# Kernel optimization log

Measured on AMD Instinct MI355X. Metric: run time of the kernel, lower is better.

## Reference

```python
import jax, jax.numpy as jnp
import numpy as np

N, D = 4096, 512
TAU, ALPHA, EPS = 0.2, 0.5, 1e-15
L2_EPS = 1e-12  # F.normalize eps


def setup_inputs() -> dict:
    key = jax.random.key(0)
    ks = jax.random.split(key, 12)
    # xavier_normal_ with gain=1.414 for [D, D] linears
    std = 1.414 * (2.0 / (D + D)) ** 0.5
    xn = lambda k: jax.random.normal(k, (D, D), jnp.float32) * std
    return {
        "z1": jax.random.normal(ks[0], (N, D), jnp.float32),
        "z2": jax.random.normal(ks[1], (N, D), jnp.float32),
        # local projector: Linear -> PReLU -> Linear
        "lw1": xn(ks[2]), "lb1": jnp.zeros((D,), jnp.float32),
        "la": jnp.full((1,), 0.25, jnp.float32),  # PReLU weight (torch default 0.25)
        "lw2": xn(ks[3]), "lb2": jnp.zeros((D,), jnp.float32),
        # global projector
        "gw1": xn(ks[4]), "gb1": jnp.zeros((D,), jnp.float32),
        "ga": jnp.full((1,), 0.25, jnp.float32),
        "gw2": xn(ks[5]), "gb2": jnp.zeros((D,), jnp.float32),
        # discriminator bilinear weight
        "W": xn(ks[6]),
        # binary positive-pair mask [N, N]
        "mask": jax.random.randint(ks[7], (N, N), 0, 2, jnp.int32),
    }


def _prelu(x, a):
    return jnp.where(x >= 0, x, a * x)


def _proj(z, w1, b1, a, w2, b2):
    # nn.Sequential(Linear, PReLU, Linear); torch Linear: z @ W.T + b
    return _prelu(z @ w1.T + b1, a[0]) @ w2.T + b2


def _l2norm(z):
    n = jnp.linalg.norm(z, axis=-1, keepdims=True)
    return z / jnp.maximum(n, L2_EPS)


def _infonce(h1, h2, m, tau):
    a = _l2norm(h1)
    b = _l2norm(h2)
    sim_intra = jnp.exp(a @ a.T / tau)  # [N, N]
    sim_inter = jnp.exp(a @ b.T / tau)  # [N, N]
    num = (sim_inter * m).sum(1)
    den = sim_intra.sum(1) + sim_inter.sum(1) - (sim_intra * m).sum(1)
    return (-jnp.log(num / den)).mean()


def reference(z1, z2, lw1, lb1, la, lw2, lb2, gw1, gb1, ga, gw2, gb2, W, mask):
    m = mask.astype(jnp.float32)
    # local (node-level) InfoNCE through the local projector
    h1 = _proj(z1, lw1, lb1, la, lw2, lb2)
    h2 = _proj(z2, lw1, lb1, la, lw2, lb2)
    local = 0.5 * (_infonce(h1, h2, m, TAU) + _infonce(h2, h1, m.T, TAU))

    # global (DGI-style) loss
    def gloss(pos_z, neg_z):
        s = pos_z.mean(0)                               # readout [D]
        h = _proj(s, gw1, gb1, ga, gw2, gb2)            # global projector [D]
        summ = W @ h                                    # [D]
        d_pos = jax.nn.sigmoid(pos_z @ summ)            # [N]
        d_neg = jax.nn.sigmoid(neg_z @ summ)            # [N]
        pos_loss = -jnp.log(d_pos + EPS).mean()
        neg_loss = -jnp.log(1.0 - d_neg + EPS).mean()
        return 0.5 * (pos_loss + neg_loss)

    glob = 0.5 * (gloss(z1, z2) + gloss(z2, z1))
    return ALPHA * local + (1.0 - ALPHA) * glob
```

## Files before the change

kernel.cpp:

```cpp
#include <hip/hip_runtime.h>
#include <math.h>

#define NN 4096
#define DD 512
#define INV_TAU 5.0f
#define EPSV 1e-15f

typedef unsigned short u16;
typedef __attribute__((ext_vector_type(8))) short short8;
typedef __attribute__((ext_vector_type(4))) float f32x4;

__device__ __forceinline__ void gld16(const void* g, void* l) {
  __builtin_amdgcn_global_load_lds(
      (const __attribute__((address_space(1))) unsigned int*)g,
      (__attribute__((address_space(3))) unsigned int*)l, 16, 0, 0);
}

__device__ __forceinline__ void bar_vm4() {
  asm volatile("s_waitcnt vmcnt(4) lgkmcnt(0)\n\ts_barrier" ::: "memory");
}
__device__ __forceinline__ void bar_vm0() {
  asm volatile("s_waitcnt vmcnt(0) lgkmcnt(0)\n\ts_barrier" ::: "memory");
}

__device__ __forceinline__ float bf2f(u16 u) {
  return __uint_as_float(((unsigned)u) << 16);
}
__device__ __forceinline__ u16 f2bf(float x) {
  unsigned u = __float_as_uint(x);
  u += 0x7fff + ((u >> 16) & 1);
  return (u16)(u >> 16);
}

__device__ __forceinline__ float wave_sum(float v) {
#pragma unroll
  for (int o = 32; o > 0; o >>= 1) v += __shfl_down(v, o, 64);
  return v;
}

__global__ __launch_bounds__(256) void tobf16_2(const float* __restrict__ a,
                                                const float* __restrict__ b,
                                                u16* __restrict__ d,
                                                int n4each) {
  const int i = blockIdx.x * 256 + threadIdx.x;
  const float* s =
      (i < n4each) ? a + (size_t)i * 4 : b + (size_t)(i - n4each) * 4;
  float4 v = *(const float4*)s;
  unsigned long long pk = (unsigned long long)f2bf(v.x) |
                          ((unsigned long long)f2bf(v.y) << 16) |
                          ((unsigned long long)f2bf(v.z) << 32) |
                          ((unsigned long long)f2bf(v.w) << 48);
  *(unsigned long long*)&d[(size_t)i * 4] = pk;
}

template <int ACT>
__global__ __launch_bounds__(256) void gemm_mfma(
    const u16* __restrict__ A, const u16* __restrict__ Bw,
    const float* __restrict__ bias, const float* __restrict__ alpha_p,
    u16* __restrict__ out) {
  __shared__ __align__(16) u16 sh[3 * 2 * 128 * 32];
  const int tid = threadIdx.x, w = tid >> 6, lane = tid & 63;
  const int quad = lane >> 4, m16 = lane & 15;
  const int wi = w >> 1, wj = w & 1;
  const int i0 = blockIdx.y * 128, j0 = blockIdx.x * 128;
  const u16* Ab = A + (size_t)blockIdx.z * ((size_t)NN * DD);
  u16* ob = out + (size_t)blockIdx.z * ((size_t)NN * DD);
  const int roff =
      (m16 >> 1) * 64 + (((((m16 & 1) << 2) | quad) ^ (m16 >> 1)) * 8);
  const int st = (lane & 7) ^ (lane >> 3);
  const int srow = 2 * (lane >> 3) + (st >> 2);
  const int scol = (st & 3) * 8;
  const int p = w >> 1, rh = (w & 1) * 64;
  const u16* gs = p ? Bw : Ab;
  const int gr = (p ? j0 : i0) + rh + srow;
  u16* dst0 = sh + p * 4096 + rh * 32;
  auto stage = [&](int bo, int k) {
    const int kn = k * 32;
#pragma unroll
    for (int rr = 0; rr < 64; rr += 16)
      gld16(&gs[(size_t)(gr + rr) * DD + kn + scol], dst0 + bo + rr * 32);
  };
  stage(0, 0);
  stage(8192, 1);
  bar_vm4();
  f32x4 acc[4][4] = {};
  int ro = 0;
  for (int kc = 0; kc < 16; ++kc) {
    if (kc <= 13) {
      int so = ro + 16384;
      if (so >= 24576) so -= 24576;
      stage(so, kc + 2);
    }
    const u16* As = sh + ro;
    const u16* Bs = sh + ro + 4096;
    short8 ar[4], br[4];
#pragma unroll
    for (int s = 0; s < 4; ++s) {
      ar[s] = *(const short8*)&As[(wi * 64 + s * 16) * 32 + roff];
      br[s] = *(const short8*)&Bs[(wj * 64 + s * 16) * 32 + roff];
    }
    __builtin_amdgcn_s_setprio(1);
#pragma unroll
    for (int si = 0; si < 4; ++si)
#pragma unroll
      for (int sj = 0; sj < 4; ++sj)
        acc[si][sj] = __builtin_amdgcn_mfma_f32_16x16x32_bf16(
            ar[si], br[sj], acc[si][sj], 0, 0, 0);
    __builtin_amdgcn_s_setprio(0);
    if (kc <= 13) bar_vm4();
    else if (kc == 14) bar_vm0();
    ro += 8192;
    if (ro == 24576) ro = 0;
  }
  const float al = ACT ? alpha_p[0] : 0.f;
#pragma unroll
  for (int si = 0; si < 4; ++si)
#pragma unroll
    for (int sj = 0; sj < 4; ++sj) {
      const int col = j0 + wj * 64 + sj * 16 + m16;
      const float bv = bias[col];
#pragma unroll
      for (int r = 0; r < 4; ++r) {
        const int row = i0 + wi * 64 + si * 16 + quad * 4 + r;
        float x = acc[si][sj][r] + bv;
        if (ACT) x = (x >= 0.f) ? x : al * x;
        ob[(size_t)row * DD + col] = f2bf(x);
      }
    }
}

__global__ __launch_bounds__(256) void rownorm_bf16(const u16* __restrict__ h,
                                                    u16* __restrict__ o) {
  const int row = blockIdx.x;
  const int t = threadIdx.x;
  const size_t base = (size_t)row * DD;
  float v0 = bf2f(h[base + t]);
  float v1 = bf2f(h[base + 256 + t]);
  float s = v0 * v0 + v1 * v1;
  s = wave_sum(s);
  __shared__ float wsum[4];
  const int lane = t & 63, wid = t >> 6;
  if (lane == 0) wsum[wid] = s;
  __syncthreads();
  if (t == 0) {
    float tot = wsum[0] + wsum[1] + wsum[2] + wsum[3];
    wsum[0] = 1.f / fmaxf(sqrtf(tot), 1e-12f);
  }
  __syncthreads();
  const float inv = wsum[0];
  o[base + t] = f2bf(v0 * inv);
  o[base + 256 + t] = f2bf(v1 * inv);
}

__global__ __launch_bounds__(512) void sim_mfma(
    const u16* __restrict__ na, const u16* __restrict__ nb,
    const int* __restrict__ mask, float* __restrict__ zb) {
  extern __shared__ __align__(16) u16 shm[];
  const int tid = threadIdx.x;
  const int w = tid >> 6, lane = tid & 63;
  const int quad = lane >> 4, m16 = lane & 15;
  const int ig = w & 3, jh = w >> 2;
  const int i0 = blockIdx.y * 128, j0 = blockIdx.x * 128;
  const int roff =
      (m16 >> 1) * 64 + (((((m16 & 1) << 2) | quad) ^ (m16 >> 1)) * 8);
  const int st = (lane & 7) ^ (lane >> 3);
  const int srow = 2 * (lane >> 3) + (st >> 2);
  const int scol = (st & 3) * 8;
  const int p = w >> 1, rh = (w & 1) * 64;
  const u16* gs = (p & 1) ? nb : na;
  const int gr = ((p < 2) ? i0 : j0) + rh + srow;
  u16* dst0 = shm + p * 4096 + rh * 32;
  auto stage = [&](int bo, int k) {
    const int kn = k * 32;
#pragma unroll
    for (int rr = 0; rr < 64; rr += 16)
      gld16(&gs[(size_t)(gr + rr) * DD + kn + scol], dst0 + bo + rr * 32);
  };
  stage(0, 0);
  stage(16384, 1);
  bar_vm4();
  f32x4 a11[2][4] = {}, a12[2][4] = {}, a22[2][4] = {};
  int ro = 0;
  for (int kc = 0; kc < 16; ++kc) {
    if (kc <= 13) {
      int so = ro + 32768;
      if (so >= 49152) so -= 49152;
      stage(so, kc + 2);
    }
    const u16* Ai = shm + ro;
    const u16* Bi = shm + ro + 4096;
    const u16* Aj = shm + ro + 8192;
    const u16* Bj = shm + ro + 12288;
    short8 ai0 = *(const short8*)&Ai[(ig * 32) * 32 + roff];
    short8 ai1 = *(const short8*)&Ai[(ig * 32 + 16) * 32 + roff];
    short8 bi0 = *(const short8*)&Bi[(ig * 32) * 32 + roff];
    short8 bi1 = *(const short8*)&Bi[(ig * 32 + 16) * 32 + roff];
#pragma unroll
    for (int c = 0; c < 4; ++c) {
      short8 aj = *(const short8*)&Aj[(jh * 64 + c * 16) * 32 + roff];
      short8 bj = *(const short8*)&Bj[(jh * 64 + c * 16) * 32 + roff];
      __builtin_amdgcn_s_setprio(1);
      a11[0][c] = __builtin_amdgcn_mfma_f32_16x16x32_bf16(ai0, aj, a11[0][c], 0, 0, 0);
      a11[1][c] = __builtin_amdgcn_mfma_f32_16x16x32_bf16(ai1, aj, a11[1][c], 0, 0, 0);
      a12[0][c] = __builtin_amdgcn_mfma_f32_16x16x32_bf16(ai0, bj, a12[0][c], 0, 0, 0);
      a12[1][c] = __builtin_amdgcn_mfma_f32_16x16x32_bf16(ai1, bj, a12[1][c], 0, 0, 0);
      a22[0][c] = __builtin_amdgcn_mfma_f32_16x16x32_bf16(bi0, bj, a22[0][c], 0, 0, 0);
      a22[1][c] = __builtin_amdgcn_mfma_f32_16x16x32_bf16(bi1, bj, a22[1][c], 0, 0, 0);
      __builtin_amdgcn_s_setprio(0);
    }
    if (kc <= 13) bar_vm4();
    else if (kc == 14) bar_vm0();
    ro += 16384;
    if (ro == 49152) ro = 0;
  }
  float* rred = (float*)(shm + 16384);
  float* cred = rred + 512;
  rred[tid] = 0.f;
  rred[tid + 512] = 0.f;
  __syncthreads();
  float rs11[2][4] = {}, rm11[2][4] = {}, rs12[2][4] = {}, rm12[2][4] = {};
  float cs12[4] = {}, cm12[4] = {}, cs22[4] = {}, cm22[4] = {};
#pragma unroll
  for (int t = 0; t < 2; ++t)
#pragma unroll
    for (int c = 0; c < 4; ++c) {
      const int gj = j0 + jh * 64 + c * 16 + m16;
#pragma unroll
      for (int r = 0; r < 4; ++r) {
        const int gi = i0 + ig * 32 + t * 16 + quad * 4 + r;
        const float mv = (float)mask[(size_t)gi * NN + gj];
        const float e11 = __expf(a11[t][c][r] * INV_TAU);
        const float e12 = __expf(a12[t][c][r] * INV_TAU);
        const float e22 = __expf(a22[t][c][r] * INV_TAU);
        rs11[t][r] += e11;
        rm11[t][r] += e11 * mv;
        rs12[t][r] += e12;
        rm12[t][r] += e12 * mv;
        cs12[c] += e12;
        cm12[c] += e12 * mv;
        cs22[c] += e22;
        cm22[c] += e22 * mv;
      }
    }
#pragma unroll
  for (int t = 0; t < 2; ++t)
#pragma unroll
    for (int r = 0; r < 4; ++r) {
      float v0 = rs11[t][r], v1 = rm11[t][r], v2 = rs12[t][r], v3 = rm12[t][r];
#pragma unroll
      for (int o = 1; o < 16; o <<= 1) {
        v0 += __shfl_xor(v0, o, 64);
        v1 += __shfl_xor(v1, o, 64);
        v2 += __shfl_xor(v2, o, 64);
        v3 += __shfl_xor(v3, o, 64);
      }
      if (m16 == 0) {
        const int il = ig * 32 + t * 16 + quad * 4 + r;
        atomicAdd(&rred[0 * 128 + il], v0);
        atomicAdd(&rred[1 * 128 + il], v1);
        atomicAdd(&rred[2 * 128 + il], v2);
        atomicAdd(&rred[3 * 128 + il], v3);
      }
    }
#pragma unroll
  for (int c = 0; c < 4; ++c) {
    float v0 = cs12[c], v1 = cm12[c], v2 = cs22[c], v3 = cm22[c];
    v0 += __shfl_xor(v0, 16, 64); v0 += __shfl_xor(v0, 32, 64);
    v1 += __shfl_xor(v1, 16, 64); v1 += __shfl_xor(v1, 32, 64);
    v2 += __shfl_xor(v2, 16, 64); v2 += __shfl_xor(v2, 32, 64);
    v3 += __shfl_xor(v3, 16, 64); v3 += __shfl_xor(v3, 32, 64);
    if (lane < 16) {
      const int jl = jh * 64 + c * 16 + lane;
      atomicAdd(&cred[0 * 128 + jl], v0);
      atomicAdd(&cred[1 * 128 + jl], v1);
      atomicAdd(&cred[2 * 128 + jl], v2);
      atomicAdd(&cred[3 * 128 + jl], v3);
    }
  }
  __syncthreads();
  if (tid < 128) {
#pragma unroll
    for (int q = 0; q < 4; ++q)
      atomicAdd(&zb[q * NN + i0 + tid], rred[q * 128 + tid]);
  } else if (tid < 256) {
    const int jl = tid - 128;
#pragma unroll
    for (int q = 0; q < 4; ++q)
      atomicAdd(&zb[(4 + q) * NN + j0 + jl], cred[q * 128 + jl]);
  }
}

__global__ __launch_bounds__(256) void local_fin(const float* __restrict__ zb,
                                                 float* __restrict__ scal) {
  const int i = blockIdx.x * 256 + threadIdx.x;
  const float r11 = zb[i], r11m = zb[NN + i];
  const float r12 = zb[2 * NN + i], r12m = zb[3 * NN + i];
  const float c12 = zb[4 * NN + i], c12m = zb[5 * NN + i];
  const float c22 = zb[6 * NN + i], c22m = zb[7 * NN + i];
  float l1 = -logf(r12m / (r11 + r12 - r11m));
  float l2 = -logf(c12m / (c22 + c12 - c22m));
  l1 = wave_sum(l1);
  l2 = wave_sum(l2);
  __shared__ float b1[4], b2[4];
  const int lane = threadIdx.x & 63, wid = threadIdx.x >> 6;
  if (lane == 0) { b1[wid] = l1; b2[wid] = l2; }
  __syncthreads();
  if (threadIdx.x == 0) {
    atomicAdd(&scal[0], b1[0] + b1[1] + b1[2] + b1[3]);
    atomicAdd(&scal[1], b2[0] + b2[1] + b2[2] + b2[3]);
  }
}

__global__ __launch_bounds__(256) void colmean(const float* __restrict__ z1,
                                               const float* __restrict__ z2,
                                               float* __restrict__ s1,
                                               float* __restrict__ s2) {
  const int c = blockIdx.x * 256 + threadIdx.x;
  const int r0 = blockIdx.y * 64;
  float a = 0.f, b = 0.f;
  for (int r = r0; r < r0 + 64; ++r) {
    a += z1[(size_t)r * DD + c];
    b += z2[(size_t)r * DD + c];
  }
  atomicAdd(&s1[c], a * (1.f / NN));
  atomicAdd(&s2[c], b * (1.f / NN));
}

__global__ __launch_bounds__(256) void matvec2(
    const float* __restrict__ M, const float* __restrict__ x1,
    const float* __restrict__ x2, const float* __restrict__ bias,
    const float* __restrict__ alpha_p, int act, float* __restrict__ y1,
    float* __restrict__ y2) {
  const float* x = blockIdx.y ? x2 : x1;
  float* y = blockIdx.y ? y2 : y1;
  const int row = (blockIdx.x * 256 + threadIdx.x) >> 6;
  const int lane = threadIdx.x & 63;
  float acc = 0.f;
#pragma unroll
  for (int t = 0; t < 8; ++t)
    acc = fmaf(M[(size_t)row * DD + lane + 64 * t], x[lane + 64 * t], acc);
  acc = wave_sum(acc);
  if (lane == 0) {
    if (bias) acc += bias[row];
    if (act) { const float al = alpha_p[0]; acc = (acc >= 0.f) ? acc : al * acc; }
    y[row] = acc;
  }
}

__global__ __launch_bounds__(256) void logsig2(
    const float* __restrict__ z1, const float* __restrict__ z2,
    const float* __restrict__ sm1, const float* __restrict__ sm2,
    float* __restrict__ scal) {
  const int ch = blockIdx.y;
  const float* z = ch ? z2 : z1;
  const float* sp = ch ? sm2 : sm1;
  const float* sn = ch ? sm1 : sm2;
  float* accP = ch ? &scal[4] : &scal[2];
  float* accN = ch ? &scal[3] : &scal[5];
  const int lane = threadIdx.x & 63;
  const int wid = threadIdx.x >> 6;
  const int row = blockIdx.x * 4 + wid;
  float dp = 0.f, dn = 0.f;
#pragma unroll
  for (int t = 0; t < 8; ++t) {
    const float zv = z[(size_t)row * DD + lane + 64 * t];
    dp = fmaf(zv, sp[lane + 64 * t], dp);
    dn = fmaf(zv, sn[lane + 64 * t], dn);
  }
  dp = wave_sum(dp);
  dn = wave_sum(dn);
  __shared__ float bp[4], bn[4];
  if (lane == 0) {
    const float sg = 1.f / (1.f + __expf(-dp));
    bp[wid] = -logf(sg + EPSV);
    const float sg2 = 1.f / (1.f + __expf(-dn));
    bn[wid] = -logf(1.f - sg2 + EPSV);
  }
  __syncthreads();
  if (threadIdx.x == 0) {
    atomicAdd(accP, bp[0] + bp[1] + bp[2] + bp[3]);
    atomicAdd(accN, bn[0] + bn[1] + bn[2] + bn[3]);
  }
}

__global__ void combine(const float* __restrict__ scal, float* __restrict__ out) {
  const float local = 0.5f * (scal[0] + scal[1]) * (1.f / NN);
  const float glob = 0.25f * (scal[2] + scal[3] + scal[4] + scal[5]) * (1.f / NN);
  out[0] = 0.5f * local + 0.5f * glob;
}

extern "C" void kernel_launch(void* const* d_in, const int* in_sizes, int n_in,
                              void* d_out, int out_size, void* d_ws,
                              size_t ws_size, hipStream_t stream) {
  const float* z1 = (const float*)d_in[0];
  const float* z2 = (const float*)d_in[1];
  const float* lw1 = (const float*)d_in[2];
  const float* lb1 = (const float*)d_in[3];
  const float* la = (const float*)d_in[4];
  const float* lw2 = (const float*)d_in[5];
  const float* lb2 = (const float*)d_in[6];
  const float* gw1 = (const float*)d_in[7];
  const float* gb1 = (const float*)d_in[8];
  const float* ga = (const float*)d_in[9];
  const float* gw2 = (const float*)d_in[10];
  const float* gb2 = (const float*)d_in[11];
  const float* W = (const float*)d_in[12];
  const int* mask = (const int*)d_in[13];
  float* out = (float*)d_out;

  static bool attr_set = false;
  if (!attr_set) {
    (void)hipFuncSetAttribute(reinterpret_cast<const void*>(sim_mfma),
                              hipFuncAttributeMaxDynamicSharedMemorySize,
                              98304);
    attr_set = true;
  }

  const size_t ND = (size_t)NN * DD;
  u16* W1b = (u16*)d_ws;
  u16* W2b = W1b + 512 * 512;
  u16* Ab = W1b + 2 * 512 * 512;
  u16* Bb = Ab + 2 * ND;
  float* zbf = (float*)(Bb + 2 * ND);
  float* s1 = zbf + 8 * NN;
  float* s2 = s1 + DD;
  float* scal = s2 + DD;
  float* t1 = scal + 16;
  float* hg1 = t1 + DD;
  float* summ1 = hg1 + DD;
  float* t2 = summ1 + DD;
  float* hg2 = t2 + DD;
  float* summ2 = hg2 + DD;

  hipMemsetAsync(zbf, 0, (8 * NN + 2 * DD + 16) * sizeof(float), stream);

  dim3 blk(256);
  tobf16_2<<<512, blk, 0, stream>>>(lw1, lw2, W1b, 512 * 512 / 4);
  tobf16_2<<<4096, blk, 0, stream>>>(z1, z2, Ab, (int)(ND / 4));

  dim3 gg(4, 32, 2);
  gemm_mfma<1><<<gg, blk, 0, stream>>>(Ab, W1b, lb1, la, Bb);
  gemm_mfma<0><<<gg, blk, 0, stream>>>(Bb, W2b, lb2, la, Ab);
  rownorm_bf16<<<2 * NN, blk, 0, stream>>>(Ab, Bb);

  sim_mfma<<<dim3(NN / 128, NN / 128), dim3(512), 98304, stream>>>(
      Bb, Bb + ND, mask, zbf);
  local_fin<<<NN / 256, blk, 0, stream>>>(zbf, scal);

  colmean<<<dim3(DD / 256, 64), blk, 0, stream>>>(z1, z2, s1, s2);
  matvec2<<<dim3(DD / 4, 2), blk, 0, stream>>>(gw1, s1, s2, gb1, ga, 1, t1, t2);
  matvec2<<<dim3(DD / 4, 2), blk, 0, stream>>>(gw2, t1, t2, gb2, nullptr, 0, hg1, hg2);
  matvec2<<<dim3(DD / 4, 2), blk, 0, stream>>>(W, hg1, hg2, nullptr, nullptr, 0, summ1, summ2);
  logsig2<<<dim3(NN / 4, 2), blk, 0, stream>>>(z1, z2, summ1, summ2, scal);

  combine<<<1, 1, 0, stream>>>(scal, out);
}
```

Baseline: 310.2 us.

## Merge conversions, retile projector GEMM, fuse tail into cooperative kernel

Merges the two bf16 conversion launches into one and retiles the projector GEMM to 128x64 tiles with 512 threads and an XCD-aware block mapping. Row normalisation now uses one wave per row with vector loads. The memset is replaced by zeroing inside rownorm and sim_mfma. The global-loss tail (column mean, three matvecs, log-sigmoid, combine) and local_fin become one cooperative kernel with grid syncs, with the old launches kept as a fallback. The goal is fewer launches and better GEMM occupancy; the costs are grid-sync overhead and reliance on ordering between kernels for the zeroing to be correct.

```diff
diff --git a/kernel.cpp b/kernel.cpp
--- a/kernel.cpp
+++ b/kernel.cpp
@@ -1,5 +1,8 @@
 #include <hip/hip_runtime.h>
+#include <hip/hip_cooperative_groups.h>
 #include <math.h>
+
+namespace cg = cooperative_groups;
 
 #define NN 4096
 #define DD 512
@@ -19,6 +22,12 @@
 __device__ __forceinline__ void bar_vm4() {
   asm volatile("s_waitcnt vmcnt(4) lgkmcnt(0)\n\ts_barrier" ::: "memory");
 }
+__device__ __forceinline__ void bar_vm2() {
+  asm volatile("s_waitcnt vmcnt(2) lgkmcnt(0)\n\ts_barrier" ::: "memory");
+}
+__device__ __forceinline__ void bar_vm1() {
+  asm volatile("s_waitcnt vmcnt(1) lgkmcnt(0)\n\ts_barrier" ::: "memory");
+}
 __device__ __forceinline__ void bar_vm0() {
   asm volatile("s_waitcnt vmcnt(0) lgkmcnt(0)\n\ts_barrier" ::: "memory");
 }
@@ -38,90 +47,112 @@
   return v;
 }
 
-__global__ __launch_bounds__(256) void tobf16_2(const float* __restrict__ a,
-                                                const float* __restrict__ b,
-                                                u16* __restrict__ d,
-                                                int n4each) {
+__global__ __launch_bounds__(256) void tobf16_4(
+    const float* __restrict__ a, const float* __restrict__ b,
+    const float* __restrict__ c, const float* __restrict__ d2,
+    u16* __restrict__ o, int na, int nb, int nc) {
   const int i = blockIdx.x * 256 + threadIdx.x;
-  const float* s =
-      (i < n4each) ? a + (size_t)i * 4 : b + (size_t)(i - n4each) * 4;
+  int j = i;
+  const float* s;
+  if (j < na) {
+    s = a + (size_t)j * 4;
+  } else {
+    j -= na;
+    if (j < nb) {
+      s = b + (size_t)j * 4;
+    } else {
+      j -= nb;
+      if (j < nc) {
+        s = c + (size_t)j * 4;
+      } else {
+        j -= nc;
+        s = d2 + (size_t)j * 4;
+      }
+    }
+  }
   float4 v = *(const float4*)s;
   unsigned long long pk = (unsigned long long)f2bf(v.x) |
                           ((unsigned long long)f2bf(v.y) << 16) |
                           ((unsigned long long)f2bf(v.z) << 32) |
                           ((unsigned long long)f2bf(v.w) << 48);
-  *(unsigned long long*)&d[(size_t)i * 4] = pk;
+  *(unsigned long long*)&o[(size_t)i * 4] = pk;
 }
 
 template <int ACT>
-__global__ __launch_bounds__(256) void gemm_mfma(
+__global__ __launch_bounds__(512) void gemm_mfma(
     const u16* __restrict__ A, const u16* __restrict__ Bw,
     const float* __restrict__ bias, const float* __restrict__ alpha_p,
     u16* __restrict__ out) {
-  __shared__ __align__(16) u16 sh[3 * 2 * 128 * 32];
+  __shared__ __align__(16) u16 sh[3 * 6144];
   const int tid = threadIdx.x, w = tid >> 6, lane = tid & 63;
   const int quad = lane >> 4, m16 = lane & 15;
   const int wi = w >> 1, wj = w & 1;
-  const int i0 = blockIdx.y * 128, j0 = blockIdx.x * 128;
-  const u16* Ab = A + (size_t)blockIdx.z * ((size_t)NN * DD);
-  u16* ob = out + (size_t)blockIdx.z * ((size_t)NN * DD);
+  const int bid = blockIdx.x;
+  const int xcd = bid & 7, idx = bid >> 3;
+  const int i0 = (4 * xcd + (idx & 3)) * 128;
+  const int j0 = ((idx >> 2) & 7) * 64;
+  const int bz = idx >> 5;
+  const u16* Ab = A + (size_t)bz * ((size_t)NN * DD);
+  u16* ob = out + (size_t)bz * ((size_t)NN * DD);
   const int roff =
       (m16 >> 1) * 64 + (((((m16 & 1) << 2) | quad) ^ (m16 >> 1)) * 8);
   const int st = (lane & 7) ^ (lane >> 3);
   const int srow = 2 * (lane >> 3) + (st >> 2);
   const int scol = (st & 3) * 8;
-  const int p = w >> 1, rh = (w & 1) * 64;
-  const u16* gs = p ? Bw : Ab;
-  const int gr = (p ? j0 : i0) + rh + srow;
-  u16* dst0 = sh + p * 4096 + rh * 32;
+  const u16* gs = (w < 4) ? Ab : Bw;
+  const int grow0 = ((w < 4) ? i0 + 2 * w * 16 : j0 + (w - 4) * 16) + srow;
+  const int doff0 = (w < 4) ? 2 * w * 512 : 4096 + (w - 4) * 512;
   auto stage = [&](int bo, int k) {
     const int kn = k * 32;
-#pragma unroll
-    for (int rr = 0; rr < 64; rr += 16)
-      gld16(&gs[(size_t)(gr + rr) * DD + kn + scol], dst0 + bo + rr * 32);
+    gld16(&gs[(size_t)grow0 * DD + kn + scol], sh + bo + doff0);
+    if (w < 4)
+      gld16(&gs[(size_t)(grow0 + 16) * DD + kn + scol], sh + bo + doff0 + 512);
   };
   stage(0, 0);
-  stage(8192, 1);
-  bar_vm4();
-  f32x4 acc[4][4] = {};
+  stage(6144, 1);
+  if (w < 4) bar_vm2(); else bar_vm1();
+  f32x4 acc[2][2] = {};
   int ro = 0;
   for (int kc = 0; kc < 16; ++kc) {
     if (kc <= 13) {
-      int so = ro + 16384;
-      if (so >= 24576) so -= 24576;
+      int so = ro + 12288;
+      if (so >= 18432) so -= 18432;
       stage(so, kc + 2);
     }
     const u16* As = sh + ro;
     const u16* Bs = sh + ro + 4096;
-    short8 ar[4], br[4];
-#pragma unroll
-    for (int s = 0; s < 4; ++s) {
-      ar[s] = *(const short8*)&As[(wi * 64 + s * 16) * 32 + roff];
-      br[s] = *(const short8*)&Bs[(wj * 64 + s * 16) * 32 + roff];
+    short8 ar[2], br[2];
+#pragma unroll
+    for (int s = 0; s < 2; ++s) {
+      ar[s] = *(const short8*)&As[(wi * 32 + s * 16) * 32 + roff];
+      br[s] = *(const short8*)&Bs[(wj * 32 + s * 16) * 32 + roff];
     }
     __builtin_amdgcn_s_setprio(1);
 #pragma unroll
-    for (int si = 0; si < 4; ++si)
-#pragma unroll
-      for (int sj = 0; sj < 4; ++sj)
+    for (int si = 0; si < 2; ++si)
+#pragma unroll
+      for (int sj = 0; sj < 2; ++sj)
         acc[si][sj] = __builtin_amdgcn_mfma_f32_16x16x32_bf16(
             ar[si], br[sj], acc[si][sj], 0, 0, 0);
     __builtin_amdgcn_s_setprio(0);
-    if (kc <= 13) bar_vm4();
-    else if (kc == 14) bar_vm0();
-    ro += 8192;
-    if (ro == 24576) ro = 0;
+    if (kc <= 13) {
+      if (w < 4) bar_vm2(); else bar_vm1();
+    } else if (kc == 14) {
+      bar_vm0();
+    }
+    ro += 6144;
+    if (ro == 18432) ro = 0;
   }
   const float al = ACT ? alpha_p[0] : 0.f;
 #pragma unroll
-  for (int si = 0; si < 4; ++si)
-#pragma unroll
-    for (int sj = 0; sj < 4; ++sj) {
-      const int col = j0 + wj * 64 + sj * 16 + m16;
+  for (int si = 0; si < 2; ++si)
+#pragma unroll
+    for (int sj = 0; sj < 2; ++sj) {
+      const int col = j0 + wj * 32 + sj * 16 + m16;
       const float bv = bias[col];
 #pragma unroll
       for (int r = 0; r < 4; ++r) {
-        const int row = i0 + wi * 64 + si * 16 + quad * 4 + r;
+        const int row = i0 + wi * 32 + si * 16 + quad * 4 + r;
         float x = acc[si][sj][r] + bv;
         if (ACT) x = (x >= 0.f) ? x : al * x;
         ob[(size_t)row * DD + col] = f2bf(x);
@@ -130,33 +161,40 @@
 }
 
 __global__ __launch_bounds__(256) void rownorm_bf16(const u16* __restrict__ h,
-                                                    u16* __restrict__ o) {
-  const int row = blockIdx.x;
-  const int t = threadIdx.x;
-  const size_t base = (size_t)row * DD;
-  float v0 = bf2f(h[base + t]);
-  float v1 = bf2f(h[base + 256 + t]);
-  float s = v0 * v0 + v1 * v1;
+                                                    u16* __restrict__ o,
+                                                    float* __restrict__ zbf) {
+  const int tid = threadIdx.x;
+  if (blockIdx.x < 128) zbf[blockIdx.x * 256 + tid] = 0.f;
+  const int row = blockIdx.x * 4 + (tid >> 6);
+  const int lane = tid & 63;
+  const size_t base = (size_t)row * DD + lane * 8;
+  short8 v = *(const short8*)&h[base];
+  float f[8];
+  float s = 0.f;
+#pragma unroll
+  for (int j = 0; j < 8; ++j) {
+    f[j] = bf2f((u16)v[j]);
+    s += f[j] * f[j];
+  }
   s = wave_sum(s);
-  __shared__ float wsum[4];
-  const int lane = t & 63, wid = t >> 6;
-  if (lane == 0) wsum[wid] = s;
-  __syncthreads();
-  if (t == 0) {
-    float tot = wsum[0] + wsum[1] + wsum[2] + wsum[3];
-    wsum[0] = 1.f / fmaxf(sqrtf(tot), 1e-12f);
-  }
-  __syncthreads();
-  const float inv = wsum[0];
-  o[base + t] = f2bf(v0 * inv);
-  o[base + 256 + t] = f2bf(v1 * inv);
+  const float inv = 1.f / fmaxf(sqrtf(__shfl(s, 0, 64)), 1e-12f);
+  short8 r;
+#pragma unroll
+  for (int j = 0; j < 8; ++j) r[j] = (short)f2bf(f[j] * inv);
+  *(short8*)&o[base] = r;
 }
 
 __global__ __launch_bounds__(512) void sim_mfma(
     const u16* __restrict__ na, const u16* __restrict__ nb,
-    const int* __restrict__ mask, float* __restrict__ zb) {
+    const int* __restrict__ mask, float* __restrict__ zb,
+    float* __restrict__ sclr) {
   extern __shared__ __align__(16) u16 shm[];
   const int tid = threadIdx.x;
+  if (blockIdx.x == 0 && blockIdx.y == 0) {
+    sclr[tid] = 0.f;
+    sclr[tid + 512] = 0.f;
+    if (tid < 16) sclr[1024 + tid] = 0.f;
+  }
   const int w = tid >> 6, lane = tid & 63;
   const int quad = lane >> 4, m16 = lane & 15;
   const int ig = w & 3, jh = w >> 2;
@@ -191,7 +229,8 @@
     const u16* Bi = shm + ro + 4096;
     const u16* Aj = shm + ro + 8192;
     const u16* Bj = shm + ro + 12288;
-    short8 ai0 = *(const short8*)&Ai[(ig * 32) * 32 + roff];
+    short8 ai0 = *(const short8*)&Ai[(ig * 32 + m16) * 32 + roff - m16 * 32 + 0];
+    ai0 = *(const short8*)&Ai[(ig * 32) * 32 + roff];
     short8 ai1 = *(const short8*)&Ai[(ig * 32 + 16) * 32 + roff];
     short8 bi0 = *(const short8*)&Bi[(ig * 32) * 32 + roff];
     short8 bi1 = *(const short8*)&Bi[(ig * 32 + 16) * 32 + roff];
@@ -290,40 +329,169 @@
   }
 }
 
-__global__ __launch_bounds__(256) void local_fin(const float* __restrict__ zb,
-                                                 float* __restrict__ scal) {
-  const int i = blockIdx.x * 256 + threadIdx.x;
-  const float r11 = zb[i], r11m = zb[NN + i];
-  const float r12 = zb[2 * NN + i], r12m = zb[3 * NN + i];
-  const float c12 = zb[4 * NN + i], c12m = zb[5 * NN + i];
-  const float c22 = zb[6 * NN + i], c22m = zb[7 * NN + i];
-  float l1 = -logf(r12m / (r11 + r12 - r11m));
-  float l2 = -logf(c12m / (c22 + c12 - c22m));
-  l1 = wave_sum(l1);
-  l2 = wave_sum(l2);
-  __shared__ float b1[4], b2[4];
-  const int lane = threadIdx.x & 63, wid = threadIdx.x >> 6;
-  if (lane == 0) { b1[wid] = l1; b2[wid] = l2; }
-  __syncthreads();
-  if (threadIdx.x == 0) {
-    atomicAdd(&scal[0], b1[0] + b1[1] + b1[2] + b1[3]);
-    atomicAdd(&scal[1], b2[0] + b2[1] + b2[2] + b2[3]);
-  }
-}
-
-__global__ __launch_bounds__(256) void colmean(const float* __restrict__ z1,
-                                               const float* __restrict__ z2,
-                                               float* __restrict__ s1,
-                                               float* __restrict__ s2) {
-  const int c = blockIdx.x * 256 + threadIdx.x;
-  const int r0 = blockIdx.y * 64;
-  float a = 0.f, b = 0.f;
-  for (int r = r0; r < r0 + 64; ++r) {
-    a += z1[(size_t)r * DD + c];
-    b += z2[(size_t)r * DD + c];
-  }
-  atomicAdd(&s1[c], a * (1.f / NN));
-  atomicAdd(&s2[c], b * (1.f / NN));
+__global__ __launch_bounds__(256) void tail_coop(
+    const float* __restrict__ zb, const float* __restrict__ z1,
+    const float* __restrict__ z2, const float* __restrict__ gw1,
+    const float* __restrict__ gb1, const float* __restrict__ ga,
+    const float* __restrict__ gw2, const float* __restrict__ gb2,
+    const float* __restrict__ W, float* __restrict__ s1,
+    float* __restrict__ s2, float* __restrict__ t1, float* __restrict__ t2,
+    float* __restrict__ hg1, float* __restrict__ hg2,
+    float* __restrict__ sm1, float* __restrict__ sm2,
+    float* __restrict__ scal, float* __restrict__ out) {
+  cg::grid_group grid = cg::this_grid();
+  const int b = blockIdx.x, tid = threadIdx.x;
+  const int lane = tid & 63, wid = tid >> 6;
+  __shared__ float red[8], b1s[4], b2s[4];
+  {
+    float a0 = 0.f, a1 = 0.f, c0 = 0.f, c1 = 0.f;
+    const int r0 = b * 16;
+    for (int r = r0; r < r0 + 16; ++r) {
+      const size_t ro = (size_t)r * DD;
+      a0 += z1[ro + tid];
+      a1 += z1[ro + 256 + tid];
+      c0 += z2[ro + tid];
+      c1 += z2[ro + 256 + tid];
+    }
+    atomicAdd(&s1[tid], a0 * (1.f / NN));
+    atomicAdd(&s1[tid + 256], a1 * (1.f / NN));
+    atomicAdd(&s2[tid], c0 * (1.f / NN));
+    atomicAdd(&s2[tid + 256], c1 * (1.f / NN));
+  }
+  if (b >= 64 && b < 80) {
+    const int i = (b - 64) * 256 + tid;
+    const float r11 = zb[i], r11m = zb[NN + i];
+    const float r12 = zb[2 * NN + i], r12m = zb[3 * NN + i];
+    const float c12 = zb[4 * NN + i], c12m = zb[5 * NN + i];
+    const float c22 = zb[6 * NN + i], c22m = zb[7 * NN + i];
+    float l1 = -logf(r12m / (r11 + r12 - r11m));
+    float l2 = -logf(c12m / (c22 + c12 - c22m));
+    l1 = wave_sum(l1);
+    l2 = wave_sum(l2);
+    if (lane == 0) { b1s[wid] = l1; b2s[wid] = l2; }
+    __syncthreads();
+    if (tid == 0) {
+      atomicAdd(&scal[0], b1s[0] + b1s[1] + b1s[2] + b1s[3]);
+      atomicAdd(&scal[1], b2s[0] + b2s[1] + b2s[2] + b2s[3]);
+    }
+  }
+  grid.sync();
+  const int gw = b * 4 + wid;
+  const int row = gw & 511, bt = gw >> 9;
+  {
+    const float* x = bt ? s2 : s1;
+    float* y = bt ? t2 : t1;
+    float acc = 0.f;
+#pragma unroll
+    for (int t = 0; t < 8; ++t)
+      acc = fmaf(gw1[(size_t)row * DD + lane + 64 * t], x[lane + 64 * t], acc);
+    acc = wave_sum(acc);
+    if (lane == 0) {
+      acc += gb1[row];
+      const float al = ga[0];
+      y[row] = (acc >= 0.f) ? acc : al * acc;
+    }
+  }
+  grid.sync();
+  {
+    const float* x = bt ? t2 : t1;
+    float* y = bt ? hg2 : hg1;
+    float acc = 0.f;
+#pragma unroll
+    for (int t = 0; t < 8; ++t)
+      acc = fmaf(gw2[(size_t)row * DD + lane + 64 * t], x[lane + 64 * t], acc);
+    acc = wave_sum(acc);
+    if (lane == 0) y[row] = acc + gb2[row];
+  }
+  grid.sync();
+  {
+    const float* x = bt ? hg2 : hg1;
+    float* y = bt ? sm2 : sm1;
+    float acc = 0.f;
+#pragma unroll
+    for (int t = 0; t < 8; ++t)
+      acc = fmaf(W[(size_t)row * DD + lane + 64 * t], x[lane + 64 * t], acc);
+    acc = wave_sum(acc);
+    if (lane == 0) y[row] = acc;
+  }
+  grid.sync();
+  {
+    const float* z = bt ? z2 : z1;
+    const float* sp = bt ? sm2 : sm1;
+    const float* sn = bt ? sm1 : sm2;
+    float lp = 0.f, ln_ = 0.f;
+#pragma unroll
+    for (int k = 0; k < 8; ++k) {
+      const int rr = row + 512 * k;
+      float dp = 0.f, dn = 0.f;
+#pragma unroll
+      for (int t = 0; t < 8; ++t) {
+        const float zv = z[(size_t)rr * DD + lane + 64 * t];
+        dp = fmaf(zv, sp[lane + 64 * t], dp);
+        dn = fmaf(zv, sn[lane + 64 * t], dn);
+      }
+      dp = wave_sum(dp);
+      dn = wave_sum(dn);
+      if (lane == 0) {
+        lp += -logf(1.f / (1.f + __expf(-dp)) + EPSV);
+        ln_ += -logf(1.f - 1.f / (1.f + __expf(-dn)) + EPSV);
+      }
+    }
+    if (lane == 0) { red[wid] = lp; red[4 + wid] = ln_; }
+    __syncthreads();
+    if (tid == 0) {
+      atomicAdd(bt ? &scal[4] : &scal[2], red[0] + red[1] + red[2] + red[3]);
+      atomicAdd(bt ? &scal[3] : &scal[5], red[4] + red[5] + red[6] + red[7]);
+    }
+  }
+  grid.sync();
+  if (b == 0 && tid == 0) {
+    const float local = 0.5f * (scal[0] + scal[1]) * (1.f / NN);
+    const float glob =
+        0.25f * (scal[2] + scal[3] + scal[4] + scal[5]) * (1.f / NN);
+    out[0] = 0.5f * local + 0.5f * glob;
+  }
+}
+
+__global__ __launch_bounds__(256) void k_lfcm(const float* __restrict__ zb,
+                                              const float* __restrict__ z1,
+                                              const float* __restrict__ z2,
+                                              float* __restrict__ s1,
+                                              float* __restrict__ s2,
+                                              float* __restrict__ scal) {
+  const int b = blockIdx.x, tid = threadIdx.x;
+  const int lane = tid & 63, wid = tid >> 6;
+  __shared__ float b1s[4], b2s[4];
+  float a0 = 0.f, a1 = 0.f, c0 = 0.f, c1 = 0.f;
+  const int r0 = b * 16;
+  for (int r = r0; r < r0 + 16; ++r) {
+    const size_t ro = (size_t)r * DD;
+    a0 += z1[ro + tid];
+    a1 += z1[ro + 256 + tid];
+    c0 += z2[ro + tid];
+    c1 += z2[ro + 256 + tid];
+  }
+  atomicAdd(&s1[tid], a0 * (1.f / NN));
+  atomicAdd(&s1[tid + 256], a1 * (1.f / NN));
+  atomicAdd(&s2[tid], c0 * (1.f / NN));
+  atomicAdd(&s2[tid + 256], c1 * (1.f / NN));
+  if (b >= 64 && b < 80) {
+    const int i = (b - 64) * 256 + tid;
+    const float r11 = zb[i], r11m = zb[NN + i];
+    const float r12 = zb[2 * NN + i], r12m = zb[3 * NN + i];
+    const float c12 = zb[4 * NN + i], c12m = zb[5 * NN + i];
+    const float c22 = zb[6 * NN + i], c22m = zb[7 * NN + i];
+    float l1 = -logf(r12m / (r11 + r12 - r11m));
+    float l2 = -logf(c12m / (c22 + c12 - c22m));
+    l1 = wave_sum(l1);
+    l2 = wave_sum(l2);
+    if (lane == 0) { b1s[wid] = l1; b2s[wid] = l2; }
+    __syncthreads();
+    if (tid == 0) {
+      atomicAdd(&scal[0], b1s[0] + b1s[1] + b1s[2] + b1s[3]);
+      atomicAdd(&scal[1], b2s[0] + b2s[1] + b2s[2] + b2s[3]);
+    }
+  }
 }
 
 __global__ __launch_bounds__(256) void matvec2(
@@ -432,26 +600,37 @@
   float* hg2 = t2 + DD;
   float* summ2 = hg2 + DD;
 
-  hipMemsetAsync(zbf, 0, (8 * NN + 2 * DD + 16) * sizeof(float), stream);
-
-  dim3 blk(256);
-  tobf16_2<<<512, blk, 0, stream>>>(lw1, lw2, W1b, 512 * 512 / 4);
-  tobf16_2<<<4096, blk, 0, stream>>>(z1, z2, Ab, (int)(ND / 4));
-
-  dim3 gg(4, 32, 2);
-  gemm_mfma<1><<<gg, blk, 0, stream>>>(Ab, W1b, lb1, la, Bb);
-  gemm_mfma<0><<<gg, blk, 0, stream>>>(Bb, W2b, lb2, la, Ab);
-  rownorm_bf16<<<2 * NN, blk, 0, stream>>>(Ab, Bb);
-
+  tobf16_4<<<4608, dim3(256), 0, stream>>>(lw1, lw2, z1, z2, W1b, 65536, 65536,
+                                           524288);
+  gemm_mfma<1><<<512, dim3(512), 0, stream>>>(Ab, W1b, lb1, la, Bb);
+  gemm_mfma<0><<<512, dim3(512), 0, stream>>>(Bb, W2b, lb2, la, Ab);
+  rownorm_bf16<<<2048, dim3(256), 0, stream>>>(Ab, Bb, zbf);
   sim_mfma<<<dim3(NN / 128, NN / 128), dim3(512), 98304, stream>>>(
-      Bb, Bb + ND, mask, zbf);
-  local_fin<<<NN / 256, blk, 0, stream>>>(zbf, scal);
-
-  colmean<<<dim3(DD / 256, 64), blk, 0, stream>>>(z1, z2, s1, s2);
-  matvec2<<<dim3(DD / 4, 2), blk, 0, stream>>>(gw1, s1, s2, gb1, ga, 1, t1, t2);
-  matvec2<<<dim3(DD / 4, 2), blk, 0, stream>>>(gw2, t1, t2, gb2, nullptr, 0, hg1, hg2);
-  matvec2<<<dim3(DD / 4, 2), blk, 0, stream>>>(W, hg1, hg2, nullptr, nullptr, 0, summ1, summ2);
-  logsig2<<<dim3(NN / 4, 2), blk, 0, stream>>>(z1, z2, summ1, summ2, scal);
-
-  combine<<<1, 1, 0, stream>>>(scal, out);
-}
+      Bb, Bb + ND, mask, zbf, s1);
+  {
+    void* args[19];
+    args[0] = (void*)&zbf;  args[1] = (void*)&z1;   args[2] = (void*)&z2;
+    args[3] = (void*)&gw1;  args[4] = (void*)&gb1;  args[5] = (void*)&ga;
+    args[6] = (void*)&gw2;  args[7] = (void*)&gb2;  args[8] = (void*)&W;
+    args[9] = (void*)&s1;   args[10] = (void*)&s2;  args[11] = (void*)&t1;
+    args[12] = (void*)&t2;  args[13] = (void*)&hg1; args[14] = (void*)&hg2;
+    args[15] = (void*)&summ1; args[16] = (void*)&summ2;
+    args[17] = (void*)&scal; args[18] = (void*)&out;
+    hipError_t ce = hipLaunchCooperativeKernel(
+        reinterpret_cast<const void*>(tail_coop), dim3(256), dim3(256), args,
+        0, stream);
+    if (ce != hipSuccess) {
+      (void)hipGetLastError();
+      k_lfcm<<<256, dim3(256), 0, stream>>>(zbf, z1, z2, s1, s2, scal);
+      matvec2<<<dim3(DD / 4, 2), dim3(256), 0, stream>>>(gw1, s1, s2, gb1, ga,
+                                                         1, t1, t2);
+      matvec2<<<dim3(DD / 4, 2), dim3(256), 0, stream>>>(gw2, t1, t2, gb2,
+                                                         nullptr, 0, hg1, hg2);
+      matvec2<<<dim3(DD / 4, 2), dim3(256), 0, stream>>>(
+          W, hg1, hg2, nullptr, nullptr, 0, summ1, summ2);
+      logsig2<<<dim3(NN / 4, 2), dim3(256), 0, stream>>>(z1, z2, summ1, summ2,
+                                                         scal);
+      combine<<<1, 1, 0, stream>>>(scal, out);
+    }
+  }
+}
```

After: 411.6 us. 1.33x slower.
